# Kernel tuning notes

Measured on AMD Instinct MI355X. Metric: run time of the kernel, lower is better.

The kernel has to match this reference:

```python
import jax, jax.numpy as jnp
import numpy as np

N = 8192
F = 64
OUT = 64


def setup_inputs() -> dict:
    key = jax.random.key(0)
    k1, k2, k3 = jax.random.split(key, 3)
    adj = jax.random.uniform(k1, (N, N), dtype=jnp.float32)
    features = jax.random.normal(k2, (N, F), dtype=jnp.float32)
    # torch Linear weight: [out_features, in_features*2], xavier_uniform with relu gain
    gain = float(np.sqrt(2.0))
    fan_in, fan_out = 2 * F, OUT
    bound = gain * float(np.sqrt(6.0 / (fan_in + fan_out)))
    W = jax.random.uniform(k3, (OUT, 2 * F), dtype=jnp.float32, minval=-bound, maxval=bound)
    return {"adj": adj, "features": features, "W": W}


def reference(adj, features, W):
    # neigh = (adj @ x) / (rowsum(adj) + 1)   -- dense 2D branch of SageConvLayer
    deg = jnp.sum(adj, axis=1, keepdims=True) + 1.0          # [N, 1]
    neigh = jnp.matmul(adj, features) / deg                   # [N, F]
    data = jnp.concatenate([features, neigh], axis=-1)        # [N, 2F]
    return jnp.matmul(data, W.T)                              # [N, OUT]
```

## Files before the change

kernel.cpp:

```cpp
#include <hip/hip_runtime.h>

#define NN 8192
#define FF 64
#define NOUT 64
#define KS 32
#define KCHUNK (NN / KS)

typedef __bf16 bf16x8 __attribute__((ext_vector_type(8)));
typedef float f32x4 __attribute__((ext_vector_type(4)));

__device__ inline bf16x8 cvt8(float4 a, float4 b) {
    bf16x8 r;
    r[0] = (__bf16)a.x; r[1] = (__bf16)a.y; r[2] = (__bf16)a.z; r[3] = (__bf16)a.w;
    r[4] = (__bf16)b.x; r[5] = (__bf16)b.y; r[6] = (__bf16)b.z; r[7] = (__bf16)b.w;
    return r;
}

__global__ __launch_bounds__(256)
void transpose_kernel(const float* __restrict__ feat, __bf16* __restrict__ featT) {
    __shared__ __bf16 t[64][72];
    int tid = threadIdx.x, blk = blockIdx.x;
    int r = tid >> 2, c0 = (tid & 3) * 16;
    const float* p = feat + (size_t)(blk * 64 + r) * FF + c0;
    float4 v0 = *(const float4*)(p);
    float4 v1 = *(const float4*)(p + 4);
    float4 v2 = *(const float4*)(p + 8);
    float4 v3 = *(const float4*)(p + 12);
    #pragma unroll
    for (int j = 0; j < 4; ++j) {
        t[c0 + 0 + j][r]  = (__bf16)(&v0.x)[j];
        t[c0 + 4 + j][r]  = (__bf16)(&v1.x)[j];
        t[c0 + 8 + j][r]  = (__bf16)(&v2.x)[j];
        t[c0 + 12 + j][r] = (__bf16)(&v3.x)[j];
    }
    __syncthreads();
    int n = tid >> 2, co = (tid & 3) * 16;
    __bf16* dst = featT + (size_t)n * NN + blk * 64 + co;
    *(bf16x8*)dst       = *(const bf16x8*)&t[n][co];
    *(bf16x8*)(dst + 8) = *(const bf16x8*)&t[n][co + 8];
}

__global__ __launch_bounds__(256, 4)
void main_kernel(const float* __restrict__ adj, const __bf16* __restrict__ featT,
                 __bf16* __restrict__ partN, float* __restrict__ partDeg) {
    __shared__ __bf16 bt[64][264];
    int tid = threadIdx.x;
    int w = tid >> 6, lane = tid & 63, ln = lane & 15, q = lane >> 4;
    int ks = blockIdx.x & (KS - 1);
    int mt = blockIdx.x >> 5;

    {
        int n = tid >> 2, kb = (tid & 3) * 64;
        const __bf16* src = featT + (size_t)n * NN + ks * KCHUNK + kb;
        #pragma unroll
        for (int i = 0; i < 8; ++i)
            *(bf16x8*)&bt[n][kb + i * 8] = *(const bf16x8*)(src + i * 8);
    }
    __syncthreads();

    int rowA = mt * 128 + w * 32 + ln;
    const float* ap0 = adj + (size_t)rowA * NN + ks * KCHUNK + q * 8;
    const float* ap1 = ap0 + (size_t)16 * NN;

    f32x4 acc[2][4], accd[2];
    #pragma unroll
    for (int f = 0; f < 2; ++f) {
        accd[f] = 0;
        #pragma unroll
        for (int t = 0; t < 4; ++t) acc[f][t] = 0;
    }

    bf16x8 ones;
    __bf16 o = (ln == 0) ? (__bf16)1.0f : (__bf16)0.0f;
    #pragma unroll
    for (int i = 0; i < 8; ++i) ones[i] = o;

    #pragma unroll 4
    for (int s = 0; s < KCHUNK / 32; ++s) {
        float4 a0 = *(const float4*)(ap0);
        float4 a1 = *(const float4*)(ap0 + 4);
        float4 a2 = *(const float4*)(ap1);
        float4 a3 = *(const float4*)(ap1 + 4);
        bf16x8 b0 = *(const bf16x8*)&bt[ln][s * 32 + q * 8];
        bf16x8 b1 = *(const bf16x8*)&bt[ln + 16][s * 32 + q * 8];
        bf16x8 b2 = *(const bf16x8*)&bt[ln + 32][s * 32 + q * 8];
        bf16x8 b3 = *(const bf16x8*)&bt[ln + 48][s * 32 + q * 8];
        bf16x8 af0 = cvt8(a0, a1);
        bf16x8 af1 = cvt8(a2, a3);
        acc[0][0] = __builtin_amdgcn_mfma_f32_16x16x32_bf16(af0, b0, acc[0][0], 0, 0, 0);
        acc[1][0] = __builtin_amdgcn_mfma_f32_16x16x32_bf16(af1, b0, acc[1][0], 0, 0, 0);
        acc[0][1] = __builtin_amdgcn_mfma_f32_16x16x32_bf16(af0, b1, acc[0][1], 0, 0, 0);
        acc[1][1] = __builtin_amdgcn_mfma_f32_16x16x32_bf16(af1, b1, acc[1][1], 0, 0, 0);
        acc[0][2] = __builtin_amdgcn_mfma_f32_16x16x32_bf16(af0, b2, acc[0][2], 0, 0, 0);
        acc[1][2] = __builtin_amdgcn_mfma_f32_16x16x32_bf16(af1, b2, acc[1][2], 0, 0, 0);
        acc[0][3] = __builtin_amdgcn_mfma_f32_16x16x32_bf16(af0, b3, acc[0][3], 0, 0, 0);
        acc[1][3] = __builtin_amdgcn_mfma_f32_16x16x32_bf16(af1, b3, acc[1][3], 0, 0, 0);
        accd[0] = __builtin_amdgcn_mfma_f32_16x16x32_bf16(af0, ones, accd[0], 0, 0, 0);
        accd[1] = __builtin_amdgcn_mfma_f32_16x16x32_bf16(af1, ones, accd[1], 0, 0, 0);
        ap0 += 32; ap1 += 32;
    }

    #pragma unroll
    for (int f = 0; f < 2; ++f) {
        int grow = mt * 128 + w * 32 + f * 16 + q * 4;
        #pragma unroll
        for (int r = 0; r < 4; ++r) {
            size_t base = ((size_t)(ks << 13) + grow + r) * FF + ln;
            partN[base +  0] = (__bf16)acc[f][0][r];
            partN[base + 16] = (__bf16)acc[f][1][r];
            partN[base + 32] = (__bf16)acc[f][2][r];
            partN[base + 48] = (__bf16)acc[f][3][r];
        }
        if (ln == 0) {
            #pragma unroll
            for (int r = 0; r < 4; ++r)
                partDeg[(ks << 13) + grow + r] = accd[f][r];
        }
    }
}

__global__ __launch_bounds__(256)
void epilogue_kernel(const float* __restrict__ feat, const float* __restrict__ W,
                     const __bf16* __restrict__ partN, const float* __restrict__ partDeg,
                     float* __restrict__ out) {
    __shared__ __bf16 dataB[64][136];
    __shared__ float rdeg[64];
    int tid = threadIdx.x, blk = blockIdx.x;

    if (tid < 64) {
        float s = 0.f;
        #pragma unroll
        for (int ks = 0; ks < KS; ++ks) s += partDeg[(ks << 13) + blk * 64 + tid];
        rdeg[tid] = 1.0f / (s + 1.0f);
    }
    __syncthreads();

    #pragma unroll
    for (int i = 0; i < 2; ++i) {
        int idx = tid + i * 256;
        int r = idx >> 3, c = (idx & 7) * 8;
        float s[8];
        #pragma unroll
        for (int j = 0; j < 8; ++j) s[j] = 0.f;
        #pragma unroll
        for (int ks = 0; ks < KS; ++ks) {
            bf16x8 v = *(const bf16x8*)&partN[((size_t)(ks << 13) + blk * 64 + r) * FF + c];
            #pragma unroll
            for (int j = 0; j < 8; ++j) s[j] += (float)v[j];
        }
        float rd = rdeg[r];
        bf16x8 o;
        #pragma unroll
        for (int j = 0; j < 8; ++j) o[j] = (__bf16)(s[j] * rd);
        *(bf16x8*)&dataB[r][64 + c] = o;
    }
    #pragma unroll
    for (int i = 0; i < 2; ++i) {
        int idx = tid + i * 256;
        int r = idx >> 3, c = (idx & 7) * 8;
        const float* p = feat + (size_t)(blk * 64 + r) * FF + c;
        float4 f0 = *(const float4*)p;
        float4 f1 = *(const float4*)(p + 4);
        *(bf16x8*)&dataB[r][c] = cvt8(f0, f1);
    }
    __syncthreads();

    int w = tid >> 6, lane = tid & 63, ln = lane & 15, q = lane >> 4;
    f32x4 acc[4];
    #pragma unroll
    for (int t = 0; t < 4; ++t) acc[t] = 0;

    #pragma unroll
    for (int kk = 0; kk < 4; ++kk) {
        bf16x8 af = *(const bf16x8*)&dataB[w * 16 + ln][kk * 32 + q * 8];
        #pragma unroll
        for (int t = 0; t < 4; ++t) {
            const float* wp = W + (size_t)(t * 16 + ln) * 128 + kk * 32 + q * 8;
            float4 b0 = *(const float4*)wp;
            float4 b1 = *(const float4*)(wp + 4);
            bf16x8 bf = cvt8(b0, b1);
            acc[t] = __builtin_amdgcn_mfma_f32_16x16x32_bf16(af, bf, acc[t], 0, 0, 0);
        }
    }

    int grow = blk * 64 + w * 16 + q * 4;
    #pragma unroll
    for (int t = 0; t < 4; ++t)
        #pragma unroll
        for (int r = 0; r < 4; ++r)
            out[(size_t)(grow + r) * NOUT + t * 16 + ln] = acc[t][r];
}

extern "C" void kernel_launch(void* const* d_in, const int* in_sizes, int n_in,
                              void* d_out, int out_size, void* d_ws, size_t ws_size,
                              hipStream_t stream) {
    const float* adj  = (const float*)d_in[0];
    const float* feat = (const float*)d_in[1];
    const float* W    = (const float*)d_in[2];
    float* out = (float*)d_out;
    char* ws = (char*)d_ws;

    __bf16* featT   = (__bf16*)ws;
    __bf16* partN   = (__bf16*)(ws + (1 << 20));
    float*  partDeg = (float*)(ws + (1 << 20) + (size_t)KS * NN * FF * 2);

    transpose_kernel<<<NN / 64, 256, 0, stream>>>(feat, featT);
    main_kernel<<<(NN / 128) * KS, 256, 0, stream>>>(adj, featT, partN, partDeg);
    epilogue_kernel<<<NN / 64, 256, 0, stream>>>(feat, W, partN, partDeg, out);
}
```

Before: 380.9 us.

## Fuse feature transpose into main kernel and halve K-split count

The separate transpose kernel is removed. Each main-kernel block now loads its fp32 feature chunk directly, converts it to bf16 and transposes it into shared memory. The K-split is reduced from 32 to 16, so each block covers a 512-wide chunk with a padded LDS tile, and launch bounds are lowered to 2 blocks per SM. This removes one launch and halves the partial-sum traffic the epilogue has to read. The cost is larger LDS use, lower occupancy, fewer blocks, and strided scalar LDS writes during the transpose.

```diff
diff --git a/kernel.cpp b/kernel.cpp
--- a/kernel.cpp
+++ b/kernel.cpp
@@ -3,8 +3,10 @@
 #define NN 8192
 #define FF 64
 #define NOUT 64
-#define KS 32
+#define KS 16
 #define KCHUNK (NN / KS)
+#define PAD 8
+#define BSTRIDE (KCHUNK + PAD)
 
 typedef __bf16 bf16x8 __attribute__((ext_vector_type(8)));
 typedef float f32x4 __attribute__((ext_vector_type(4)));
@@ -16,45 +18,34 @@
     return r;
 }
 
-__global__ __launch_bounds__(256)
-void transpose_kernel(const float* __restrict__ feat, __bf16* __restrict__ featT) {
-    __shared__ __bf16 t[64][72];
-    int tid = threadIdx.x, blk = blockIdx.x;
-    int r = tid >> 2, c0 = (tid & 3) * 16;
-    const float* p = feat + (size_t)(blk * 64 + r) * FF + c0;
-    float4 v0 = *(const float4*)(p);
-    float4 v1 = *(const float4*)(p + 4);
-    float4 v2 = *(const float4*)(p + 8);
-    float4 v3 = *(const float4*)(p + 12);
-    #pragma unroll
-    for (int j = 0; j < 4; ++j) {
-        t[c0 + 0 + j][r]  = (__bf16)(&v0.x)[j];
-        t[c0 + 4 + j][r]  = (__bf16)(&v1.x)[j];
-        t[c0 + 8 + j][r]  = (__bf16)(&v2.x)[j];
-        t[c0 + 12 + j][r] = (__bf16)(&v3.x)[j];
-    }
-    __syncthreads();
-    int n = tid >> 2, co = (tid & 3) * 16;
-    __bf16* dst = featT + (size_t)n * NN + blk * 64 + co;
-    *(bf16x8*)dst       = *(const bf16x8*)&t[n][co];
-    *(bf16x8*)(dst + 8) = *(const bf16x8*)&t[n][co + 8];
-}
-
-__global__ __launch_bounds__(256, 4)
-void main_kernel(const float* __restrict__ adj, const __bf16* __restrict__ featT,
+__global__ __launch_bounds__(256, 2)
+void main_kernel(const float* __restrict__ adj, const float* __restrict__ feat,
                  __bf16* __restrict__ partN, float* __restrict__ partDeg) {
-    __shared__ __bf16 bt[64][264];
+    __shared__ __bf16 bt[64][BSTRIDE];
     int tid = threadIdx.x;
     int w = tid >> 6, lane = tid & 63, ln = lane & 15, q = lane >> 4;
     int ks = blockIdx.x & (KS - 1);
-    int mt = blockIdx.x >> 5;
+    int mt = blockIdx.x >> 4;
 
     {
-        int n = tid >> 2, kb = (tid & 3) * 64;
-        const __bf16* src = featT + (size_t)n * NN + ks * KCHUNK + kb;
+        int r = tid >> 2, cg = (tid & 3) * 16;
+        const float* fb = feat + ((size_t)ks * KCHUNK + r) * FF + cg;
         #pragma unroll
-        for (int i = 0; i < 8; ++i)
-            *(bf16x8*)&bt[n][kb + i * 8] = *(const bf16x8*)(src + i * 8);
+        for (int kb = 0; kb < 8; ++kb) {
+            const float* p = fb + (size_t)kb * 64 * FF;
+            float4 v0 = *(const float4*)(p);
+            float4 v1 = *(const float4*)(p + 4);
+            float4 v2 = *(const float4*)(p + 8);
+            float4 v3 = *(const float4*)(p + 12);
+            int kk = kb * 64 + r;
+            #pragma unroll
+            for (int j = 0; j < 4; ++j) {
+                bt[cg + 0 + j][kk]  = (__bf16)(&v0.x)[j];
+                bt[cg + 4 + j][kk]  = (__bf16)(&v1.x)[j];
+                bt[cg + 8 + j][kk]  = (__bf16)(&v2.x)[j];
+                bt[cg + 12 + j][kk] = (__bf16)(&v3.x)[j];
+            }
+        }
     }
     __syncthreads();
 
@@ -200,11 +191,9 @@
     float* out = (float*)d_out;
     char* ws = (char*)d_ws;
 
-    __bf16* featT   = (__bf16*)ws;
-    __bf16* partN   = (__bf16*)(ws + (1 << 20));
-    float*  partDeg = (float*)(ws + (1 << 20) + (size_t)KS * NN * FF * 2);
+    __bf16* partN   = (__bf16*)ws;
+    float*  partDeg = (float*)(ws + (size_t)KS * NN * FF * 2);
 
-    transpose_kernel<<<NN / 64, 256, 0, stream>>>(feat, featT);
-    main_kernel<<<(NN / 128) * KS, 256, 0, stream>>>(adj, featT, partN, partDeg);
+    main_kernel<<<(NN / 128) * KS, 256, 0, stream>>>(adj, feat, partN, partDeg);
     epilogue_kernel<<<NN / 64, 256, 0, stream>>>(feat, W, partN, partDeg, out);
 }
```

Result: no change. 376.7 us (-1.1%).
